# Performance work log

Measured on AMD Instinct MI355X. Metric: run time of the kernel, lower is better.

## Reference

```python
import jax, jax.numpy as jnp
import numpy as np

K = 8               # config.k
X_MIN = -1.0        # x_min
X_MAX = 1.0         # x_max
GLOBAL_COEFF = 1.0  # config.global_coeff
EPS = 1e-8          # torch cosine_similarity eps
BZ, P, D = 8192, 1024, 1024  # batch, num_pool, data_dim


def setup_inputs() -> dict:
    key = jax.random.key(0)
    k1, k2, k3, k4, k5 = jax.random.split(key, 5)
    return {
        "ppg": jax.random.normal(k1, (BZ, 1, D), dtype=jnp.float32),
        "keys_pool": jax.random.normal(k2, (P, D), dtype=jnp.float32),
        "prompt_pool": jax.random.normal(k3, (P, D), dtype=jnp.float32),
        "cnn_w": jax.random.normal(k4, (1, 1, 3), dtype=jnp.float32) * 0.5,
        "cnn_b": jax.random.normal(k5, (1,), dtype=jnp.float32) * 0.1,
    }


def _prompt_cnn(prompt, w, b):
    # PromptCNN: Conv1d(1,1,k=3,pad=1) + ReLU on [P, D]
    x = prompt[:, None, :]  # [P, 1, D]
    y = jax.lax.conv_general_dilated(
        x, w, window_strides=(1,), padding=((1, 1),),
        dimension_numbers=("NCH", "OIH", "NCH"))
    y = jax.nn.relu(y + b[None, :, None])
    return y[:, 0, :]  # [P, D]


def _global_normalizer(prompt, x_min, x_max):
    pmax = jnp.max(prompt, axis=-1, keepdims=True)
    pmin = jnp.min(prompt, axis=-1, keepdims=True)
    scale = (x_max - x_min) / (pmax - pmin)
    return scale * (prompt - pmin) + x_min


def reference(ppg, keys_pool, prompt_pool, cnn_w, cnn_b):
    # prompt pool through CNN
    pcnn = _prompt_cnn(prompt_pool, cnn_w, cnn_b)  # [P, D]

    # cosine similarity: ppg [bz,1,D] vs keys [P,D] -> [bz,P]
    pn = ppg[:, 0, :] / jnp.maximum(
        jnp.linalg.norm(ppg[:, 0, :], axis=-1, keepdims=True), EPS)
    kn = keys_pool / jnp.maximum(
        jnp.linalg.norm(keys_pool, axis=-1, keepdims=True), EPS)
    cos = jnp.einsum("bd,pd->bp", pn, kn)  # [bz, P]
    score_ = 1.0 - cos

    # top-k smallest distances (largest=False) -> ascending order
    neg_vals, idx = jax.lax.top_k(-score_, K)  # [bz, K]
    score = -neg_vals

    # entropy of softmax over raw scores
    logp = jax.nn.log_softmax(score_, axis=-1)
    entropy = -(jnp.exp(logp) * logp).sum(axis=-1).mean()

    # gather selected prompts, average over k, add singleton channel dim
    prompt = pcnn[idx].mean(axis=1)[:, None, :]  # [bz, 1, D]

    # min-max global normalization (glonorm=True)
    prompt = _global_normalizer(prompt, X_MIN, X_MAX)

    # additive combine (mul=False)
    prompted = ppg + GLOBAL_COEFF * prompt  # [bz, 1, D]

    return prompted, score.mean(), entropy
```

## Files before the change

### kernel.cpp

```cpp
#include <hip/hip_runtime.h>
#include <hip/hip_bf16.h>

#define BZ 8192
#define PP 1024
#define DD 1024
#define KSEL 8

typedef unsigned short u16;
typedef __attribute__((ext_vector_type(8))) short bf16x8;
typedef __attribute__((ext_vector_type(4))) float f32x4;

#define WS_INVK 0
#define WS_INVP 1024
#define WS_SCORE 9216
#define WS_ENT 17408
#define WS_IDX 25600
#define WS_BF16_BYTE 368640ull
#define WS_NEED (WS_BF16_BYTE + 2ull*16777216ull + 2ull*4194304ull)

__device__ __forceinline__ u16 f2bf(float x) {
  __hip_bfloat16 h = __float2bfloat16(x);
  return *(u16*)&h;
}
__device__ __forceinline__ float bf2f(u16 u) {
  __hip_bfloat16 h; *(u16*)&h = u;
  return __bfloat162float(h);
}
__device__ __forceinline__ void gll16(const void* g, void* l) {
  __builtin_amdgcn_global_load_lds((__attribute__((address_space(1))) void*)g,
                                   (__attribute__((address_space(3))) void*)l, 16, 0, 0);
}

__global__ __launch_bounds__(256) void convert_kernel(const float* __restrict__ ppg,
                                                      const float* __restrict__ keys,
                                                      float* __restrict__ ws) {
  u16* Ahi = (u16*)((char*)ws + WS_BF16_BYTE);
  u16* Alo = Ahi + 8388608;
  u16* Bhi = Alo + 8388608;
  u16* Blo = Bhi + 1048576;

  int blk = blockIdx.x;
  const float* src; u16 *hi, *lo; float* invdst;
  if (blk < PP) {
    src = keys + (size_t)blk * DD;
    hi = Bhi + (size_t)blk * DD; lo = Blo + (size_t)blk * DD;
    invdst = ws + WS_INVK + blk;
  } else {
    int r = blk - PP;
    src = ppg + (size_t)r * DD;
    hi = Ahi + (size_t)r * DD; lo = Alo + (size_t)r * DD;
    invdst = ws + WS_INVP + r;
  }
  int t = threadIdx.x;
  float4 v = ((const float4*)src)[t];
  float x[4] = {v.x, v.y, v.z, v.w};
  u16 h4[4], l4[4];
  float s = 0.f;
  #pragma unroll
  for (int j = 0; j < 4; ++j) {
    h4[j] = f2bf(x[j]);
    l4[j] = f2bf(x[j] - bf2f(h4[j]));
    s += x[j] * x[j];
  }
  *(ushort4*)(hi + t * 4) = *(ushort4*)h4;
  *(ushort4*)(lo + t * 4) = *(ushort4*)l4;

  __shared__ float red[4];
  #pragma unroll
  for (int o = 32; o > 0; o >>= 1) s += __shfl_down(s, o);
  if ((t & 63) == 0) red[t >> 6] = s;
  __syncthreads();
  if (t == 0) {
    float tot = red[0] + red[1] + red[2] + red[3];
    *invdst = 1.0f / fmaxf(sqrtf(tot), 1e-8f);
  }
}

#define LDS_AH 0
#define LDS_AL 8192
#define LDS_BH 16384
#define LDS_BL 24576

__global__ __launch_bounds__(256, 2) void gemm_mfma(const float* __restrict__ ws_ro,
                                                    float* __restrict__ C) {
  const u16* Ahi = (const u16*)((const char*)ws_ro + WS_BF16_BYTE);
  const u16* Alo = Ahi + 8388608;
  const u16* Bhi = Alo + 8388608;
  const u16* Blo = Bhi + 1048576;

  __shared__ u16 lds[32768];

  int t = threadIdx.x;
  int wid = t >> 6, lane = t & 63;
  int lr = lane & 15, lg = lane >> 4;

  int orig = blockIdx.x;
  int wg = (orig & 7) * 64 + (orig >> 3);
  int bm0 = (wg >> 3) * 128;
  int bn0 = (wg & 7) * 128;

  int wm = wid >> 1, wn = wid & 1;

  size_t offA[4], offB[4];
  int ldso[4];
  #pragma unroll
  for (int r = 0; r < 4; ++r) {
    int s = r * 256 + t;
    int row = s >> 3, g = s & 7;
    offA[r] = (size_t)(bm0 + row) * DD + g * 8;
    offB[r] = (size_t)(bn0 + row) * DD + g * 8;
    ldso[r] = (r * 256 + wid * 64) * 8;
  }

  f32x4 acc[4][4] = {};

  for (int kt = 0; kt < 16; ++kt) {
    int k0 = kt * 64;
    #pragma unroll
    for (int r = 0; r < 4; ++r) {
      gll16(Ahi + offA[r] + k0, &lds[LDS_AH + ldso[r]]);
      gll16(Alo + offA[r] + k0, &lds[LDS_AL + ldso[r]]);
      gll16(Bhi + offB[r] + k0, &lds[LDS_BH + ldso[r]]);
      gll16(Blo + offB[r] + k0, &lds[LDS_BL + ldso[r]]);
    }
    __syncthreads();

    #pragma unroll
    for (int kh = 0; kh < 2; ++kh) {
      bf16x8 ah[4], al[4], bh[4], bl[4];
      #pragma unroll
      for (int i = 0; i < 4; ++i) {
        int off = (wm * 64 + i * 16 + lr) * 64 + kh * 32 + lg * 8;
        ah[i] = *(const bf16x8*)&lds[LDS_AH + off];
        al[i] = *(const bf16x8*)&lds[LDS_AL + off];
      }
      #pragma unroll
      for (int j = 0; j < 4; ++j) {
        int off = (wn * 64 + j * 16 + lr) * 64 + kh * 32 + lg * 8;
        bh[j] = *(const bf16x8*)&lds[LDS_BH + off];
        bl[j] = *(const bf16x8*)&lds[LDS_BL + off];
      }
      #pragma unroll
      for (int i = 0; i < 4; ++i)
        #pragma unroll
        for (int j = 0; j < 4; ++j) {
          acc[i][j] = __builtin_amdgcn_mfma_f32_16x16x32_bf16(ah[i], bh[j], acc[i][j], 0, 0, 0);
          acc[i][j] = __builtin_amdgcn_mfma_f32_16x16x32_bf16(ah[i], bl[j], acc[i][j], 0, 0, 0);
          acc[i][j] = __builtin_amdgcn_mfma_f32_16x16x32_bf16(al[i], bh[j], acc[i][j], 0, 0, 0);
        }
    }
    __syncthreads();
  }

  const float* invP = ws_ro + WS_INVP;
  const float* invK = ws_ro + WS_INVK;
  #pragma unroll
  for (int i = 0; i < 4; ++i) {
    #pragma unroll
    for (int q = 0; q < 4; ++q) {
      int row = bm0 + wm * 64 + i * 16 + lg * 4 + q;
      float ip = invP[row];
      #pragma unroll
      for (int j = 0; j < 4; ++j) {
        int col = bn0 + wn * 64 + j * 16 + lr;
        C[(size_t)row * PP + col] = acc[i][j][q] * ip * invK[col];
      }
    }
  }
}

__global__ __launch_bounds__(256) void norms_kernel(const float* __restrict__ ppg,
                                                    const float* __restrict__ keys,
                                                    float* __restrict__ ws) {
  int blk = blockIdx.x;
  const float* src; float* dst;
  if (blk < PP) { src = keys + (size_t)blk * DD; dst = ws + WS_INVK + blk; }
  else          { src = ppg + (size_t)(blk - PP) * DD; dst = ws + WS_INVP + (blk - PP); }
  int t = threadIdx.x;
  float4 v = ((const float4*)src)[t];
  float s = v.x*v.x + v.y*v.y + v.z*v.z + v.w*v.w;
  __shared__ float red[4];
  #pragma unroll
  for (int o = 32; o > 0; o >>= 1) s += __shfl_down(s, o);
  if ((t & 63) == 0) red[t >> 6] = s;
  __syncthreads();
  if (t == 0) {
    float tot = red[0] + red[1] + red[2] + red[3];
    *dst = 1.0f / fmaxf(sqrtf(tot), 1e-8f);
  }
}

#define BM 128
#define BN 128
#define BK 16
__global__ __launch_bounds__(256) void gemm_kernel(const float* __restrict__ A,
                                                   const float* __restrict__ B,
                                                   const float* __restrict__ ws,
                                                   float* __restrict__ C) {
  __shared__ float As[BK][BM];
  __shared__ float Bs[BK][BN];
  int t = threadIdx.x;
  int bm0 = (blockIdx.x / (PP / BN)) * BM;
  int bn0 = (blockIdx.x % (PP / BN)) * BN;
  int tx = t & 15, ty = t >> 4;
  float acc[8][8] = {};
  int r = t & 127;
  const float* src = (t < 128) ? (A + (size_t)(bm0 + r) * DD)
                               : (B + (size_t)(bn0 + r) * DD);
  float* dstbase = (t < 128) ? &As[0][0] : &Bs[0][0];
  for (int k0 = 0; k0 < DD; k0 += BK) {
    #pragma unroll
    for (int q = 0; q < 4; ++q) {
      float4 v = *(const float4*)(src + k0 + q * 4);
      dstbase[(q * 4 + 0) * 128 + r] = v.x;
      dstbase[(q * 4 + 1) * 128 + r] = v.y;
      dstbase[(q * 4 + 2) * 128 + r] = v.z;
      dstbase[(q * 4 + 3) * 128 + r] = v.w;
    }
    __syncthreads();
    #pragma unroll
    for (int kk = 0; kk < BK; ++kk) {
      float a[8], b[8];
      *(float4*)&a[0] = *(const float4*)&As[kk][ty * 8];
      *(float4*)&a[4] = *(const float4*)&As[kk][ty * 8 + 4];
      *(float4*)&b[0] = *(const float4*)&Bs[kk][tx * 8];
      *(float4*)&b[4] = *(const float4*)&Bs[kk][tx * 8 + 4];
      #pragma unroll
      for (int i = 0; i < 8; ++i)
        #pragma unroll
        for (int j = 0; j < 8; ++j)
          acc[i][j] = fmaf(a[i], b[j], acc[i][j]);
    }
    __syncthreads();
  }
  const float* invK = ws + WS_INVK;
  const float* invP = ws + WS_INVP;
  #pragma unroll
  for (int i = 0; i < 8; ++i) {
    int row = bm0 + ty * 8 + i;
    float ia = invP[row];
    #pragma unroll
    for (int j = 0; j < 8; j += 4) {
      int col = bn0 + tx * 8 + j;
      float4 o;
      o.x = acc[i][j + 0] * ia * invK[col + 0];
      o.y = acc[i][j + 1] * ia * invK[col + 1];
      o.z = acc[i][j + 2] * ia * invK[col + 2];
      o.w = acc[i][j + 3] * ia * invK[col + 3];
      *(float4*)(C + (size_t)row * PP + col) = o;
    }
  }
}

__global__ __launch_bounds__(256) void topk_wave_kernel(const float* __restrict__ cosm,
                                                        float* __restrict__ ws) {
  int wid = threadIdx.x >> 6, lane = threadIdx.x & 63;
  int row = blockIdx.x * 4 + wid;
  const float* crow = cosm + (size_t)row * PP;

  float c[16];
  #pragma unroll
  for (int p = 0; p < 4; ++p) {
    float4 v = *(const float4*)(crow + p * 256 + lane * 4);
    c[p * 4 + 0] = v.x; c[p * 4 + 1] = v.y; c[p * 4 + 2] = v.z; c[p * 4 + 3] = v.w;
  }

  float mn = c[0];
  #pragma unroll
  for (int l = 1; l < 16; ++l) mn = fminf(mn, c[l]);
  #pragma unroll
  for (int o = 1; o < 64; o <<= 1) mn = fminf(mn, __shfl_xor(mn, o));
  float m = 1.0f - mn;

  float z = 0.f, w = 0.f;
  #pragma unroll
  for (int l = 0; l < 16; ++l) {
    float s = 1.0f - c[l];
    float e = expf(s - m);
    z += e;
    w += s * e;
  }
  #pragma unroll
  for (int o = 1; o < 64; o <<= 1) { z += __shfl_xor(z, o); w += __shfl_xor(w, o); }
  if (lane == 0) ws[WS_ENT + row] = m + logf(z) - w / z;

  unsigned used = 0;
  float score_sum = 0.f;
  int myidx = 0;
  #pragma unroll
  for (int it = 0; it < KSEL; ++it) {
    float v = -2.0f; int gi = 1 << 30;
    #pragma unroll
    for (int l = 0; l < 16; ++l) {
      if (!((used >> l) & 1u)) {
        float cv = c[l];
        int g = ((l >> 2) << 8) | (lane << 2) | (l & 3);
        if (cv > v || (cv == v && g < gi)) { v = cv; gi = g; }
      }
    }
    #pragma unroll
    for (int o = 1; o < 64; o <<= 1) {
      float ov = __shfl_xor(v, o);
      int og = __shfl_xor(gi, o);
      if (ov > v || (ov == v && og < gi)) { v = ov; gi = og; }
    }
    score_sum += 1.0f - v;
    if (((gi >> 2) & 63) == lane) used |= 1u << ((((gi >> 8) & 3) << 2) | (gi & 3));
    if (lane == it) myidx = gi;
  }
  if (lane == 0) ws[WS_SCORE + row] = score_sum;
  if (lane < KSEL) ((int*)(ws + WS_IDX))[row * KSEL + lane] = myidx;
}

__global__ __launch_bounds__(256) void prompt_kernel(const float* __restrict__ ppg,
                                                     const float* __restrict__ pool,
                                                     const float* __restrict__ cw,
                                                     const float* __restrict__ cb,
                                                     const float* __restrict__ ws,
                                                     float* __restrict__ out) {
  int row = blockIdx.x;
  int t = threadIdx.x;
  const int* idx = (const int*)(ws + WS_IDX) + row * KSEL;
  float w0 = cw[0], w1 = cw[1], w2 = cw[2], bb = cb[0];
  int d0 = t * 4;

  float a0 = 0.f, a1 = 0.f, a2 = 0.f, a3 = 0.f;
  #pragma unroll
  for (int j = 0; j < KSEL; ++j) {
    int r = idx[j];
    const float* src = pool + (size_t)r * DD;
    float4 x = *(const float4*)(src + d0);
    float xm = (d0 > 0) ? src[d0 - 1] : 0.f;
    float xp = (d0 + 4 < DD) ? src[d0 + 4] : 0.f;
    float y0 = fmaf(w0, xm,  fmaf(w1, x.x, fmaf(w2, x.y, bb)));
    float y1 = fmaf(w0, x.x, fmaf(w1, x.y, fmaf(w2, x.z, bb)));
    float y2 = fmaf(w0, x.y, fmaf(w1, x.z, fmaf(w2, x.w, bb)));
    float y3 = fmaf(w0, x.z, fmaf(w1, x.w, fmaf(w2, xp, bb)));
    a0 += fmaxf(y0, 0.f);
    a1 += fmaxf(y1, 0.f);
    a2 += fmaxf(y2, 0.f);
    a3 += fmaxf(y3, 0.f);
  }
  float p0 = a0 * 0.125f, p1 = a1 * 0.125f, p2 = a2 * 0.125f, p3 = a3 * 0.125f;

  __shared__ float rmin[4], rmax[4];
  float lmin = fminf(fminf(p0, p1), fminf(p2, p3));
  float lmax = fmaxf(fmaxf(p0, p1), fmaxf(p2, p3));
  #pragma unroll
  for (int o = 32; o > 0; o >>= 1) {
    lmin = fminf(lmin, __shfl_down(lmin, o));
    lmax = fmaxf(lmax, __shfl_down(lmax, o));
  }
  if ((t & 63) == 0) { rmin[t >> 6] = lmin; rmax[t >> 6] = lmax; }
  __syncthreads();
  float pmin = fminf(fminf(rmin[0], rmin[1]), fminf(rmin[2], rmin[3]));
  float pmax = fmaxf(fmaxf(rmax[0], rmax[1]), fmaxf(rmax[2], rmax[3]));
  float scale = 2.0f / (pmax - pmin);

  float4 pv = *(const float4*)(ppg + (size_t)row * DD + d0);
  float4 o;
  o.x = pv.x + (scale * (p0 - pmin) - 1.0f);
  o.y = pv.y + (scale * (p1 - pmin) - 1.0f);
  o.z = pv.z + (scale * (p2 - pmin) - 1.0f);
  o.w = pv.w + (scale * (p3 - pmin) - 1.0f);
  *(float4*)(out + (size_t)row * DD + d0) = o;
}

__global__ __launch_bounds__(256) void finalize_kernel(const float* __restrict__ ws,
                                                       float* __restrict__ out) {
  int t = threadIdx.x;
  const float* ss = ws + WS_SCORE;
  const float* ee = ws + WS_ENT;
  float s = 0.f, e = 0.f;
  for (int i = t; i < BZ; i += 256) { s += ss[i]; e += ee[i]; }
  __shared__ float rs[4], re[4];
  #pragma unroll
  for (int o = 32; o > 0; o >>= 1) { s += __shfl_down(s, o); e += __shfl_down(e, o); }
  if ((t & 63) == 0) { rs[t >> 6] = s; re[t >> 6] = e; }
  __syncthreads();
  if (t == 0) {
    float sT = rs[0] + rs[1] + rs[2] + rs[3];
    float eT = re[0] + re[1] + re[2] + re[3];
    out[(size_t)BZ * DD + 0] = sT / (float)(BZ * KSEL);
    out[(size_t)BZ * DD + 1] = eT / (float)BZ;
  }
}

extern "C" void kernel_launch(void* const* d_in, const int* in_sizes, int n_in,
                              void* d_out, int out_size, void* d_ws, size_t ws_size,
                              hipStream_t stream) {
  const float* ppg  = (const float*)d_in[0];
  const float* keys = (const float*)d_in[1];
  const float* pool = (const float*)d_in[2];
  const float* cw   = (const float*)d_in[3];
  const float* cb   = (const float*)d_in[4];
  float* out = (float*)d_out;
  float* ws  = (float*)d_ws;

  if (ws_size >= WS_NEED) {
    hipLaunchKernelGGL(convert_kernel, dim3(PP + BZ), dim3(256), 0, stream, ppg, keys, ws);
    hipLaunchKernelGGL(gemm_mfma, dim3((BZ / 128) * (PP / 128)), dim3(256), 0, stream, ws, out);
  } else {
    hipLaunchKernelGGL(norms_kernel, dim3(PP + BZ), dim3(256), 0, stream, ppg, keys, ws);
    hipLaunchKernelGGL(gemm_kernel, dim3((BZ / BM) * (PP / BN)), dim3(256), 0, stream,
                       ppg, keys, ws, out);
  }
  hipLaunchKernelGGL(topk_wave_kernel, dim3(BZ / 4), dim3(256), 0, stream, out, ws);
  hipLaunchKernelGGL(prompt_kernel, dim3(BZ), dim3(256), 0, stream, ppg, pool, cw, cb, ws, out);
  hipLaunchKernelGGL(finalize_kernel, dim3(1), dim3(256), 0, stream, ws, out);
}
```

Measured before the change: 146.2 us.

## Use single fp16 MFMA GEMM with pre-normalized inputs and exact fp32 top-k refinement

Replaces the three-pass bf16 hi/lo split GEMM with one fp16 MFMA pass on rows pre-normalized in the convert kernel, and writes the cosine matrix as fp16 to workspace. The top-k kernel picks 16 candidates from the approximate scores, then recomputes their exact fp32 dot products against keys and selects the final 8. This cuts MFMA work and GEMM memory traffic by about threefold, at the cost of extra gathered key reads in the top-k step. Entropy is now computed from fp16 scores with a fixed softmax shift, which trades some accuracy. The fp32 fallback path for small workspaces is removed.

```diff
diff --git a/kernel.cpp b/kernel.cpp
--- a/kernel.cpp
+++ b/kernel.cpp
@@ -6,8 +6,9 @@
 #define DD 1024
 #define KSEL 8
 
-typedef unsigned short u16;
-typedef __attribute__((ext_vector_type(8))) short bf16x8;
+typedef _Float16 f16;
+typedef __attribute__((ext_vector_type(8))) _Float16 f16x8;
+typedef __attribute__((ext_vector_type(4))) _Float16 f16x4;
 typedef __attribute__((ext_vector_type(4))) float f32x4;
 
 #define WS_INVK 0
@@ -15,80 +16,58 @@
 #define WS_SCORE 9216
 #define WS_ENT 17408
 #define WS_IDX 25600
-#define WS_BF16_BYTE 368640ull
-#define WS_NEED (WS_BF16_BYTE + 2ull*16777216ull + 2ull*4194304ull)
-
-__device__ __forceinline__ u16 f2bf(float x) {
-  __hip_bfloat16 h = __float2bfloat16(x);
-  return *(u16*)&h;
-}
-__device__ __forceinline__ float bf2f(u16 u) {
-  __hip_bfloat16 h; *(u16*)&h = u;
-  return __bfloat162float(h);
-}
+#define WS_F16_BYTE 368640ull
+#define A16_ELEMS 8388608ull
+#define B16_ELEMS 1048576ull
+
 __device__ __forceinline__ void gll16(const void* g, void* l) {
   __builtin_amdgcn_global_load_lds((__attribute__((address_space(1))) void*)g,
                                    (__attribute__((address_space(3))) void*)l, 16, 0, 0);
 }
 
-__global__ __launch_bounds__(256) void convert_kernel(const float* __restrict__ ppg,
-                                                      const float* __restrict__ keys,
-                                                      float* __restrict__ ws) {
-  u16* Ahi = (u16*)((char*)ws + WS_BF16_BYTE);
-  u16* Alo = Ahi + 8388608;
-  u16* Bhi = Alo + 8388608;
-  u16* Blo = Bhi + 1048576;
-
-  int blk = blockIdx.x;
-  const float* src; u16 *hi, *lo; float* invdst;
+__global__ __launch_bounds__(256) void convert_f16(const float* __restrict__ ppg,
+                                                   const float* __restrict__ keys,
+                                                   float* __restrict__ ws) {
+  f16* A16 = (f16*)((char*)ws + WS_F16_BYTE);
+  f16* B16 = A16 + A16_ELEMS;
+
+  int blk = blockIdx.x, t = threadIdx.x;
+  const float* src; f16* dst; float* invdst;
   if (blk < PP) {
-    src = keys + (size_t)blk * DD;
-    hi = Bhi + (size_t)blk * DD; lo = Blo + (size_t)blk * DD;
+    src = keys + (size_t)blk * DD; dst = B16 + (size_t)blk * DD;
     invdst = ws + WS_INVK + blk;
   } else {
     int r = blk - PP;
-    src = ppg + (size_t)r * DD;
-    hi = Ahi + (size_t)r * DD; lo = Alo + (size_t)r * DD;
+    src = ppg + (size_t)r * DD; dst = A16 + (size_t)r * DD;
     invdst = ws + WS_INVP + r;
   }
-  int t = threadIdx.x;
   float4 v = ((const float4*)src)[t];
   float x[4] = {v.x, v.y, v.z, v.w};
-  u16 h4[4], l4[4];
-  float s = 0.f;
-  #pragma unroll
-  for (int j = 0; j < 4; ++j) {
-    h4[j] = f2bf(x[j]);
-    l4[j] = f2bf(x[j] - bf2f(h4[j]));
-    s += x[j] * x[j];
-  }
-  *(ushort4*)(hi + t * 4) = *(ushort4*)h4;
-  *(ushort4*)(lo + t * 4) = *(ushort4*)l4;
-
+  float s = x[0]*x[0] + x[1]*x[1] + x[2]*x[2] + x[3]*x[3];
   __shared__ float red[4];
   #pragma unroll
   for (int o = 32; o > 0; o >>= 1) s += __shfl_down(s, o);
   if ((t & 63) == 0) red[t >> 6] = s;
   __syncthreads();
-  if (t == 0) {
-    float tot = red[0] + red[1] + red[2] + red[3];
-    *invdst = 1.0f / fmaxf(sqrtf(tot), 1e-8f);
-  }
-}
-
-#define LDS_AH 0
-#define LDS_AL 8192
-#define LDS_BH 16384
-#define LDS_BL 24576
-
-__global__ __launch_bounds__(256, 2) void gemm_mfma(const float* __restrict__ ws_ro,
-                                                    float* __restrict__ C) {
-  const u16* Ahi = (const u16*)((const char*)ws_ro + WS_BF16_BYTE);
-  const u16* Alo = Ahi + 8388608;
-  const u16* Bhi = Alo + 8388608;
-  const u16* Blo = Bhi + 1048576;
-
-  __shared__ u16 lds[32768];
+  float tot = red[0] + red[1] + red[2] + red[3];
+  float inv = 1.0f / fmaxf(sqrtf(tot), 1e-8f);
+  f16x4 h;
+  #pragma unroll
+  for (int j = 0; j < 4; ++j) h[j] = (_Float16)(x[j] * inv);
+  *(f16x4*)(dst + t * 4) = h;
+  if (t == 0) *invdst = inv;
+}
+
+#define LDS_A 0
+#define LDS_B 8192
+
+__global__ __launch_bounds__(256, 2) void gemm_f16(const float* __restrict__ ws_ro,
+                                                   float* __restrict__ ws_w) {
+  const f16* A16 = (const f16*)((const char*)ws_ro + WS_F16_BYTE);
+  const f16* B16 = A16 + A16_ELEMS;
+  f16* C16 = (f16*)((char*)ws_w + WS_F16_BYTE) + A16_ELEMS + B16_ELEMS;
+
+  __shared__ unsigned short lds[16384];
 
   int t = threadIdx.x;
   int wid = t >> 6, lane = t & 63;
@@ -98,7 +77,6 @@
   int wg = (orig & 7) * 64 + (orig >> 3);
   int bm0 = (wg >> 3) * 128;
   int bn0 = (wg & 7) * 128;
-
   int wm = wid >> 1, wn = wid & 1;
 
   size_t offA[4], offB[4];
@@ -118,183 +96,81 @@
     int k0 = kt * 64;
     #pragma unroll
     for (int r = 0; r < 4; ++r) {
-      gll16(Ahi + offA[r] + k0, &lds[LDS_AH + ldso[r]]);
-      gll16(Alo + offA[r] + k0, &lds[LDS_AL + ldso[r]]);
-      gll16(Bhi + offB[r] + k0, &lds[LDS_BH + ldso[r]]);
-      gll16(Blo + offB[r] + k0, &lds[LDS_BL + ldso[r]]);
+      gll16(A16 + offA[r] + k0, &lds[LDS_A + ldso[r]]);
+      gll16(B16 + offB[r] + k0, &lds[LDS_B + ldso[r]]);
     }
     __syncthreads();
 
     #pragma unroll
     for (int kh = 0; kh < 2; ++kh) {
-      bf16x8 ah[4], al[4], bh[4], bl[4];
+      f16x8 af[4], bf[4];
       #pragma unroll
       for (int i = 0; i < 4; ++i) {
         int off = (wm * 64 + i * 16 + lr) * 64 + kh * 32 + lg * 8;
-        ah[i] = *(const bf16x8*)&lds[LDS_AH + off];
-        al[i] = *(const bf16x8*)&lds[LDS_AL + off];
+        af[i] = *(const f16x8*)&lds[LDS_A + off];
       }
       #pragma unroll
       for (int j = 0; j < 4; ++j) {
         int off = (wn * 64 + j * 16 + lr) * 64 + kh * 32 + lg * 8;
-        bh[j] = *(const bf16x8*)&lds[LDS_BH + off];
-        bl[j] = *(const bf16x8*)&lds[LDS_BL + off];
+        bf[j] = *(const f16x8*)&lds[LDS_B + off];
       }
       #pragma unroll
       for (int i = 0; i < 4; ++i)
         #pragma unroll
-        for (int j = 0; j < 4; ++j) {
-          acc[i][j] = __builtin_amdgcn_mfma_f32_16x16x32_bf16(ah[i], bh[j], acc[i][j], 0, 0, 0);
-          acc[i][j] = __builtin_amdgcn_mfma_f32_16x16x32_bf16(ah[i], bl[j], acc[i][j], 0, 0, 0);
-          acc[i][j] = __builtin_amdgcn_mfma_f32_16x16x32_bf16(al[i], bh[j], acc[i][j], 0, 0, 0);
-        }
+        for (int j = 0; j < 4; ++j)
+          acc[i][j] = __builtin_amdgcn_mfma_f32_16x16x32_f16(af[i], bf[j], acc[i][j], 0, 0, 0);
     }
     __syncthreads();
   }
 
-  const float* invP = ws_ro + WS_INVP;
-  const float* invK = ws_ro + WS_INVK;
-  #pragma unroll
-  for (int i = 0; i < 4; ++i) {
+  #pragma unroll
+  for (int i = 0; i < 4; ++i)
     #pragma unroll
     for (int q = 0; q < 4; ++q) {
       int row = bm0 + wm * 64 + i * 16 + lg * 4 + q;
-      float ip = invP[row];
       #pragma unroll
       for (int j = 0; j < 4; ++j) {
         int col = bn0 + wn * 64 + j * 16 + lr;
-        C[(size_t)row * PP + col] = acc[i][j][q] * ip * invK[col];
-      }
-    }
-  }
-}
-
-__global__ __launch_bounds__(256) void norms_kernel(const float* __restrict__ ppg,
-                                                    const float* __restrict__ keys,
-                                                    float* __restrict__ ws) {
-  int blk = blockIdx.x;
-  const float* src; float* dst;
-  if (blk < PP) { src = keys + (size_t)blk * DD; dst = ws + WS_INVK + blk; }
-  else          { src = ppg + (size_t)(blk - PP) * DD; dst = ws + WS_INVP + (blk - PP); }
-  int t = threadIdx.x;
-  float4 v = ((const float4*)src)[t];
-  float s = v.x*v.x + v.y*v.y + v.z*v.z + v.w*v.w;
-  __shared__ float red[4];
-  #pragma unroll
-  for (int o = 32; o > 0; o >>= 1) s += __shfl_down(s, o);
-  if ((t & 63) == 0) red[t >> 6] = s;
-  __syncthreads();
-  if (t == 0) {
-    float tot = red[0] + red[1] + red[2] + red[3];
-    *dst = 1.0f / fmaxf(sqrtf(tot), 1e-8f);
-  }
-}
-
-#define BM 128
-#define BN 128
-#define BK 16
-__global__ __launch_bounds__(256) void gemm_kernel(const float* __restrict__ A,
-                                                   const float* __restrict__ B,
-                                                   const float* __restrict__ ws,
-                                                   float* __restrict__ C) {
-  __shared__ float As[BK][BM];
-  __shared__ float Bs[BK][BN];
-  int t = threadIdx.x;
-  int bm0 = (blockIdx.x / (PP / BN)) * BM;
-  int bn0 = (blockIdx.x % (PP / BN)) * BN;
-  int tx = t & 15, ty = t >> 4;
-  float acc[8][8] = {};
-  int r = t & 127;
-  const float* src = (t < 128) ? (A + (size_t)(bm0 + r) * DD)
-                               : (B + (size_t)(bn0 + r) * DD);
-  float* dstbase = (t < 128) ? &As[0][0] : &Bs[0][0];
-  for (int k0 = 0; k0 < DD; k0 += BK) {
-    #pragma unroll
-    for (int q = 0; q < 4; ++q) {
-      float4 v = *(const float4*)(src + k0 + q * 4);
-      dstbase[(q * 4 + 0) * 128 + r] = v.x;
-      dstbase[(q * 4 + 1) * 128 + r] = v.y;
-      dstbase[(q * 4 + 2) * 128 + r] = v.z;
-      dstbase[(q * 4 + 3) * 128 + r] = v.w;
-    }
-    __syncthreads();
-    #pragma unroll
-    for (int kk = 0; kk < BK; ++kk) {
-      float a[8], b[8];
-      *(float4*)&a[0] = *(const float4*)&As[kk][ty * 8];
-      *(float4*)&a[4] = *(const float4*)&As[kk][ty * 8 + 4];
-      *(float4*)&b[0] = *(const float4*)&Bs[kk][tx * 8];
-      *(float4*)&b[4] = *(const float4*)&Bs[kk][tx * 8 + 4];
-      #pragma unroll
-      for (int i = 0; i < 8; ++i)
-        #pragma unroll
-        for (int j = 0; j < 8; ++j)
-          acc[i][j] = fmaf(a[i], b[j], acc[i][j]);
-    }
-    __syncthreads();
-  }
-  const float* invK = ws + WS_INVK;
-  const float* invP = ws + WS_INVP;
-  #pragma unroll
-  for (int i = 0; i < 8; ++i) {
-    int row = bm0 + ty * 8 + i;
-    float ia = invP[row];
-    #pragma unroll
-    for (int j = 0; j < 8; j += 4) {
-      int col = bn0 + tx * 8 + j;
-      float4 o;
-      o.x = acc[i][j + 0] * ia * invK[col + 0];
-      o.y = acc[i][j + 1] * ia * invK[col + 1];
-      o.z = acc[i][j + 2] * ia * invK[col + 2];
-      o.w = acc[i][j + 3] * ia * invK[col + 3];
-      *(float4*)(C + (size_t)row * PP + col) = o;
-    }
-  }
-}
-
-__global__ __launch_bounds__(256) void topk_wave_kernel(const float* __restrict__ cosm,
-                                                        float* __restrict__ ws) {
+        C16[(size_t)row * PP + col] = (_Float16)acc[i][j][q];
+      }
+    }
+}
+
+__global__ __launch_bounds__(256) void topk_refine(const float* __restrict__ ppg,
+                                                   const float* __restrict__ keys,
+                                                   float* __restrict__ ws) {
+  const f16* C16 = (const f16*)((const char*)ws + WS_F16_BYTE) + A16_ELEMS + B16_ELEMS;
   int wid = threadIdx.x >> 6, lane = threadIdx.x & 63;
   int row = blockIdx.x * 4 + wid;
-  const float* crow = cosm + (size_t)row * PP;
-
+  const f16* crow = C16 + (size_t)row * PP;
+
+  f16x8 va = *(const f16x8*)(crow + lane * 16);
+  f16x8 vb = *(const f16x8*)(crow + lane * 16 + 8);
   float c[16];
   #pragma unroll
-  for (int p = 0; p < 4; ++p) {
-    float4 v = *(const float4*)(crow + p * 256 + lane * 4);
-    c[p * 4 + 0] = v.x; c[p * 4 + 1] = v.y; c[p * 4 + 2] = v.z; c[p * 4 + 3] = v.w;
-  }
-
-  float mn = c[0];
-  #pragma unroll
-  for (int l = 1; l < 16; ++l) mn = fminf(mn, c[l]);
-  #pragma unroll
-  for (int o = 1; o < 64; o <<= 1) mn = fminf(mn, __shfl_xor(mn, o));
-  float m = 1.0f - mn;
+  for (int j = 0; j < 8; ++j) { c[j] = (float)va[j]; c[8 + j] = (float)vb[j]; }
 
   float z = 0.f, w = 0.f;
   #pragma unroll
   for (int l = 0; l < 16; ++l) {
     float s = 1.0f - c[l];
-    float e = expf(s - m);
-    z += e;
-    w += s * e;
+    float e = __expf(s - 2.0f);
+    z += e; w += s * e;
   }
   #pragma unroll
   for (int o = 1; o < 64; o <<= 1) { z += __shfl_xor(z, o); w += __shfl_xor(w, o); }
-  if (lane == 0) ws[WS_ENT + row] = m + logf(z) - w / z;
+  if (lane == 0) ws[WS_ENT + row] = 2.0f + __logf(z) - w / z;
 
   unsigned used = 0;
-  float score_sum = 0.f;
-  int myidx = 0;
-  #pragma unroll
-  for (int it = 0; it < KSEL; ++it) {
+  int cand = 0;
+  #pragma unroll
+  for (int it = 0; it < 16; ++it) {
     float v = -2.0f; int gi = 1 << 30;
     #pragma unroll
     for (int l = 0; l < 16; ++l) {
       if (!((used >> l) & 1u)) {
         float cv = c[l];
-        int g = ((l >> 2) << 8) | (lane << 2) | (l & 3);
+        int g = lane * 16 + l;
         if (cv > v || (cv == v && g < gi)) { v = cv; gi = g; }
       }
     }
@@ -304,12 +180,56 @@
       int og = __shfl_xor(gi, o);
       if (ov > v || (ov == v && og < gi)) { v = ov; gi = og; }
     }
-    score_sum += 1.0f - v;
-    if (((gi >> 2) & 63) == lane) used |= 1u << ((((gi >> 8) & 3) << 2) | (gi & 3));
-    if (lane == it) myidx = gi;
-  }
-  if (lane == 0) ws[WS_SCORE + row] = score_sum;
-  if (lane < KSEL) ((int*)(ws + WS_IDX))[row * KSEL + lane] = myidx;
+    if ((gi >> 4) == lane) used |= 1u << (gi & 15);
+    if (lane == it) cand = gi;
+  }
+
+  float p[16];
+  const float* prow = ppg + (size_t)row * DD;
+  #pragma unroll
+  for (int q = 0; q < 4; ++q) {
+    float4 pv = *(const float4*)(prow + lane * 16 + q * 4);
+    p[q * 4 + 0] = pv.x; p[q * 4 + 1] = pv.y; p[q * 4 + 2] = pv.z; p[q * 4 + 3] = pv.w;
+  }
+  float ip = ws[WS_INVP + row];
+  float rc[16]; int cd[16];
+  #pragma unroll 4
+  for (int tt = 0; tt < 16; ++tt) {
+    int bc = __shfl(cand, tt);
+    cd[tt] = bc;
+    const float* krow = keys + (size_t)bc * DD;
+    float d = 0.f;
+    #pragma unroll
+    for (int q = 0; q < 4; ++q) {
+      float4 kv = *(const float4*)(krow + lane * 16 + q * 4);
+      d = fmaf(p[q * 4 + 0], kv.x, d);
+      d = fmaf(p[q * 4 + 1], kv.y, d);
+      d = fmaf(p[q * 4 + 2], kv.z, d);
+      d = fmaf(p[q * 4 + 3], kv.w, d);
+    }
+    #pragma unroll
+    for (int o = 1; o < 64; o <<= 1) d += __shfl_xor(d, o);
+    rc[tt] = d * ip * ws[WS_INVK + bc];
+  }
+
+  unsigned u2 = 0;
+  float ssum = 0.f;
+  int mysel = 0;
+  #pragma unroll
+  for (int it = 0; it < KSEL; ++it) {
+    float bv = -2.0f; int bt = 0, bci = 1 << 30;
+    #pragma unroll
+    for (int tt = 0; tt < 16; ++tt) {
+      if (!((u2 >> tt) & 1u)) {
+        if (rc[tt] > bv || (rc[tt] == bv && cd[tt] < bci)) { bv = rc[tt]; bt = tt; bci = cd[tt]; }
+      }
+    }
+    ssum += 1.0f - bv;
+    u2 |= 1u << bt;
+    if (lane == it) mysel = bci;
+  }
+  if (lane == 0) ws[WS_SCORE + row] = ssum;
+  if (lane < KSEL) ((int*)(ws + WS_IDX))[row * KSEL + lane] = mysel;
 }
 
 __global__ __launch_bounds__(256) void prompt_kernel(const float* __restrict__ ppg,
@@ -397,15 +317,9 @@
   float* out = (float*)d_out;
   float* ws  = (float*)d_ws;
 
-  if (ws_size >= WS_NEED) {
-    hipLaunchKernelGGL(convert_kernel, dim3(PP + BZ), dim3(256), 0, stream, ppg, keys, ws);
-    hipLaunchKernelGGL(gemm_mfma, dim3((BZ / 128) * (PP / 128)), dim3(256), 0, stream, ws, out);
-  } else {
-    hipLaunchKernelGGL(norms_kernel, dim3(PP + BZ), dim3(256), 0, stream, ppg, keys, ws);
-    hipLaunchKernelGGL(gemm_kernel, dim3((BZ / BM) * (PP / BN)), dim3(256), 0, stream,
-                       ppg, keys, ws, out);
-  }
-  hipLaunchKernelGGL(topk_wave_kernel, dim3(BZ / 4), dim3(256), 0, stream, out, ws);
+  hipLaunchKernelGGL(convert_f16, dim3(PP + BZ), dim3(256), 0, stream, ppg, keys, ws);
+  hipLaunchKernelGGL(gemm_f16, dim3((BZ / 128) * (PP / 128)), dim3(256), 0, stream, ws, ws);
+  hipLaunchKernelGGL(topk_refine, dim3(BZ / 4), dim3(256), 0, stream, ppg, keys, ws);
   hipLaunchKernelGGL(prompt_kernel, dim3(BZ), dim3(256), 0, stream, ppg, pool, cw, cb, ws, out);
   hipLaunchKernelGGL(finalize_kernel, dim3(1), dim3(256), 0, stream, ws, out);
 }
```

Result: slower. 206.0 us (+40.9%).

## Fuse top-k and prompt gather into one wave-per-row kernel

Applied to the files above, without the earlier changes.

Merges the top-k/entropy kernel and the prompt CNN/normalize kernel into a single kernel where each wave handles one row and passes the selected indices by shuffle instead of through workspace memory. The entropy pass drops its row-min reduction and uses a fixed shift of 2 with fast exp/log intrinsics, which relies on cosine being at least -1. The fallback fp32 GEMM path and the workspace-size check are removed, so the MFMA path now runs unconditionally. This removes one launch and the index round trip, at the cost of more registers per wave and in-place reuse of the cos rows in out.

```diff
diff --git a/kernel.cpp b/kernel.cpp
--- a/kernel.cpp
+++ b/kernel.cpp
@@ -14,9 +14,7 @@
 #define WS_INVP 1024
 #define WS_SCORE 9216
 #define WS_ENT 17408
-#define WS_IDX 25600
 #define WS_BF16_BYTE 368640ull
-#define WS_NEED (WS_BF16_BYTE + 2ull*16777216ull + 2ull*4194304ull)
 
 __device__ __forceinline__ u16 f2bf(float x) {
   __hip_bfloat16 h = __float2bfloat16(x);
@@ -98,7 +96,6 @@
   int wg = (orig & 7) * 64 + (orig >> 3);
   int bm0 = (wg >> 3) * 128;
   int bn0 = (wg & 7) * 128;
-
   int wm = wid >> 1, wn = wid & 1;
 
   size_t offA[4], offB[4];
@@ -169,120 +166,33 @@
   }
 }
 
-__global__ __launch_bounds__(256) void norms_kernel(const float* __restrict__ ppg,
-                                                    const float* __restrict__ keys,
-                                                    float* __restrict__ ws) {
-  int blk = blockIdx.x;
-  const float* src; float* dst;
-  if (blk < PP) { src = keys + (size_t)blk * DD; dst = ws + WS_INVK + blk; }
-  else          { src = ppg + (size_t)(blk - PP) * DD; dst = ws + WS_INVP + (blk - PP); }
-  int t = threadIdx.x;
-  float4 v = ((const float4*)src)[t];
-  float s = v.x*v.x + v.y*v.y + v.z*v.z + v.w*v.w;
-  __shared__ float red[4];
-  #pragma unroll
-  for (int o = 32; o > 0; o >>= 1) s += __shfl_down(s, o);
-  if ((t & 63) == 0) red[t >> 6] = s;
-  __syncthreads();
-  if (t == 0) {
-    float tot = red[0] + red[1] + red[2] + red[3];
-    *dst = 1.0f / fmaxf(sqrtf(tot), 1e-8f);
-  }
-}
-
-#define BM 128
-#define BN 128
-#define BK 16
-__global__ __launch_bounds__(256) void gemm_kernel(const float* __restrict__ A,
-                                                   const float* __restrict__ B,
-                                                   const float* __restrict__ ws,
-                                                   float* __restrict__ C) {
-  __shared__ float As[BK][BM];
-  __shared__ float Bs[BK][BN];
-  int t = threadIdx.x;
-  int bm0 = (blockIdx.x / (PP / BN)) * BM;
-  int bn0 = (blockIdx.x % (PP / BN)) * BN;
-  int tx = t & 15, ty = t >> 4;
-  float acc[8][8] = {};
-  int r = t & 127;
-  const float* src = (t < 128) ? (A + (size_t)(bm0 + r) * DD)
-                               : (B + (size_t)(bn0 + r) * DD);
-  float* dstbase = (t < 128) ? &As[0][0] : &Bs[0][0];
-  for (int k0 = 0; k0 < DD; k0 += BK) {
-    #pragma unroll
-    for (int q = 0; q < 4; ++q) {
-      float4 v = *(const float4*)(src + k0 + q * 4);
-      dstbase[(q * 4 + 0) * 128 + r] = v.x;
-      dstbase[(q * 4 + 1) * 128 + r] = v.y;
-      dstbase[(q * 4 + 2) * 128 + r] = v.z;
-      dstbase[(q * 4 + 3) * 128 + r] = v.w;
-    }
-    __syncthreads();
-    #pragma unroll
-    for (int kk = 0; kk < BK; ++kk) {
-      float a[8], b[8];
-      *(float4*)&a[0] = *(const float4*)&As[kk][ty * 8];
-      *(float4*)&a[4] = *(const float4*)&As[kk][ty * 8 + 4];
-      *(float4*)&b[0] = *(const float4*)&Bs[kk][tx * 8];
-      *(float4*)&b[4] = *(const float4*)&Bs[kk][tx * 8 + 4];
-      #pragma unroll
-      for (int i = 0; i < 8; ++i)
-        #pragma unroll
-        for (int j = 0; j < 8; ++j)
-          acc[i][j] = fmaf(a[i], b[j], acc[i][j]);
-    }
-    __syncthreads();
-  }
-  const float* invK = ws + WS_INVK;
-  const float* invP = ws + WS_INVP;
-  #pragma unroll
-  for (int i = 0; i < 8; ++i) {
-    int row = bm0 + ty * 8 + i;
-    float ia = invP[row];
-    #pragma unroll
-    for (int j = 0; j < 8; j += 4) {
-      int col = bn0 + tx * 8 + j;
-      float4 o;
-      o.x = acc[i][j + 0] * ia * invK[col + 0];
-      o.y = acc[i][j + 1] * ia * invK[col + 1];
-      o.z = acc[i][j + 2] * ia * invK[col + 2];
-      o.w = acc[i][j + 3] * ia * invK[col + 3];
-      *(float4*)(C + (size_t)row * PP + col) = o;
-    }
-  }
-}
-
-__global__ __launch_bounds__(256) void topk_wave_kernel(const float* __restrict__ cosm,
-                                                        float* __restrict__ ws) {
+__global__ __launch_bounds__(256) void fused_wave_topk_prompt(
+    const float* __restrict__ ppg, const float* __restrict__ pool,
+    const float* __restrict__ cw, const float* __restrict__ cb,
+    float* __restrict__ ws, float* __restrict__ out) {
   int wid = threadIdx.x >> 6, lane = threadIdx.x & 63;
   int row = blockIdx.x * 4 + wid;
-  const float* crow = cosm + (size_t)row * PP;
+  const float* crow = out + (size_t)row * PP;
 
   float c[16];
   #pragma unroll
   for (int p = 0; p < 4; ++p) {
-    float4 v = *(const float4*)(crow + p * 256 + lane * 4);
-    c[p * 4 + 0] = v.x; c[p * 4 + 1] = v.y; c[p * 4 + 2] = v.z; c[p * 4 + 3] = v.w;
-  }
-
-  float mn = c[0];
-  #pragma unroll
-  for (int l = 1; l < 16; ++l) mn = fminf(mn, c[l]);
-  #pragma unroll
-  for (int o = 1; o < 64; o <<= 1) mn = fminf(mn, __shfl_xor(mn, o));
-  float m = 1.0f - mn;
-
-  float z = 0.f, w = 0.f;
-  #pragma unroll
-  for (int l = 0; l < 16; ++l) {
-    float s = 1.0f - c[l];
-    float e = expf(s - m);
-    z += e;
-    w += s * e;
-  }
-  #pragma unroll
-  for (int o = 1; o < 64; o <<= 1) { z += __shfl_xor(z, o); w += __shfl_xor(w, o); }
-  if (lane == 0) ws[WS_ENT + row] = m + logf(z) - w / z;
+    f32x4 v = *(const f32x4*)(crow + p * 256 + lane * 4);
+    c[p * 4 + 0] = v[0]; c[p * 4 + 1] = v[1]; c[p * 4 + 2] = v[2]; c[p * 4 + 3] = v[3];
+  }
+
+  {
+    float z = 0.f, w = 0.f;
+    #pragma unroll
+    for (int l = 0; l < 16; ++l) {
+      float s = 1.0f - c[l];
+      float e = __expf(s - 2.0f);
+      z += e; w += s * e;
+    }
+    #pragma unroll
+    for (int o = 1; o < 64; o <<= 1) { z += __shfl_xor(z, o); w += __shfl_xor(w, o); }
+    if (lane == 0) ws[WS_ENT + row] = 2.0f + __logf(z) - w / z;
+  }
 
   unsigned used = 0;
   float score_sum = 0.f;
@@ -309,61 +219,57 @@
     if (lane == it) myidx = gi;
   }
   if (lane == 0) ws[WS_SCORE + row] = score_sum;
-  if (lane < KSEL) ((int*)(ws + WS_IDX))[row * KSEL + lane] = myidx;
-}
-
-__global__ __launch_bounds__(256) void prompt_kernel(const float* __restrict__ ppg,
-                                                     const float* __restrict__ pool,
-                                                     const float* __restrict__ cw,
-                                                     const float* __restrict__ cb,
-                                                     const float* __restrict__ ws,
-                                                     float* __restrict__ out) {
-  int row = blockIdx.x;
-  int t = threadIdx.x;
-  const int* idx = (const int*)(ws + WS_IDX) + row * KSEL;
+
+  const float* prow = ppg + (size_t)row * DD;
+  f32x4 pv[4];
+  #pragma unroll
+  for (int j = 0; j < 4; ++j)
+    pv[j] = *(const f32x4*)(prow + j * 256 + lane * 4);
+
   float w0 = cw[0], w1 = cw[1], w2 = cw[2], bb = cb[0];
-  int d0 = t * 4;
-
-  float a0 = 0.f, a1 = 0.f, a2 = 0.f, a3 = 0.f;
-  #pragma unroll
-  for (int j = 0; j < KSEL; ++j) {
-    int r = idx[j];
-    const float* src = pool + (size_t)r * DD;
-    float4 x = *(const float4*)(src + d0);
-    float xm = (d0 > 0) ? src[d0 - 1] : 0.f;
-    float xp = (d0 + 4 < DD) ? src[d0 + 4] : 0.f;
-    float y0 = fmaf(w0, xm,  fmaf(w1, x.x, fmaf(w2, x.y, bb)));
-    float y1 = fmaf(w0, x.x, fmaf(w1, x.y, fmaf(w2, x.z, bb)));
-    float y2 = fmaf(w0, x.y, fmaf(w1, x.z, fmaf(w2, x.w, bb)));
-    float y3 = fmaf(w0, x.z, fmaf(w1, x.w, fmaf(w2, xp, bb)));
-    a0 += fmaxf(y0, 0.f);
-    a1 += fmaxf(y1, 0.f);
-    a2 += fmaxf(y2, 0.f);
-    a3 += fmaxf(y3, 0.f);
-  }
-  float p0 = a0 * 0.125f, p1 = a1 * 0.125f, p2 = a2 * 0.125f, p3 = a3 * 0.125f;
-
-  __shared__ float rmin[4], rmax[4];
-  float lmin = fminf(fminf(p0, p1), fminf(p2, p3));
-  float lmax = fmaxf(fmaxf(p0, p1), fmaxf(p2, p3));
-  #pragma unroll
-  for (int o = 32; o > 0; o >>= 1) {
-    lmin = fminf(lmin, __shfl_down(lmin, o));
-    lmax = fmaxf(lmax, __shfl_down(lmax, o));
-  }
-  if ((t & 63) == 0) { rmin[t >> 6] = lmin; rmax[t >> 6] = lmax; }
-  __syncthreads();
-  float pmin = fminf(fminf(rmin[0], rmin[1]), fminf(rmin[2], rmin[3]));
-  float pmax = fmaxf(fmaxf(rmax[0], rmax[1]), fmaxf(rmax[2], rmax[3]));
-  float scale = 2.0f / (pmax - pmin);
-
-  float4 pv = *(const float4*)(ppg + (size_t)row * DD + d0);
-  float4 o;
-  o.x = pv.x + (scale * (p0 - pmin) - 1.0f);
-  o.y = pv.y + (scale * (p1 - pmin) - 1.0f);
-  o.z = pv.z + (scale * (p2 - pmin) - 1.0f);
-  o.w = pv.w + (scale * (p3 - pmin) - 1.0f);
-  *(float4*)(out + (size_t)row * DD + d0) = o;
+  float a[16] = {};
+  #pragma unroll
+  for (int s = 0; s < KSEL; ++s) {
+    int rj = __shfl(myidx, s);
+    const float* src = pool + (size_t)rj * DD;
+    #pragma unroll
+    for (int j = 0; j < 4; ++j) {
+      int d0 = j * 256 + lane * 4;
+      f32x4 x = *(const f32x4*)(src + d0);
+      float xm = (d0 > 0) ? src[d0 - 1] : 0.f;
+      float xp = (d0 + 4 < DD) ? src[d0 + 4] : 0.f;
+      float y0 = fmaf(w0, xm,   fmaf(w1, x[0], fmaf(w2, x[1], bb)));
+      float y1 = fmaf(w0, x[0], fmaf(w1, x[1], fmaf(w2, x[2], bb)));
+      float y2 = fmaf(w0, x[1], fmaf(w1, x[2], fmaf(w2, x[3], bb)));
+      float y3 = fmaf(w0, x[2], fmaf(w1, x[3], fmaf(w2, xp,   bb)));
+      a[j * 4 + 0] += fmaxf(y0, 0.f);
+      a[j * 4 + 1] += fmaxf(y1, 0.f);
+      a[j * 4 + 2] += fmaxf(y2, 0.f);
+      a[j * 4 + 3] += fmaxf(y3, 0.f);
+    }
+  }
+  #pragma unroll
+  for (int l = 0; l < 16; ++l) a[l] *= 0.125f;
+
+  float lmin = a[0], lmax = a[0];
+  #pragma unroll
+  for (int l = 1; l < 16; ++l) { lmin = fminf(lmin, a[l]); lmax = fmaxf(lmax, a[l]); }
+  #pragma unroll
+  for (int o = 1; o < 64; o <<= 1) {
+    lmin = fminf(lmin, __shfl_xor(lmin, o));
+    lmax = fmaxf(lmax, __shfl_xor(lmax, o));
+  }
+  float scale = 2.0f / (lmax - lmin);
+
+  float* orow = out + (size_t)row * DD;
+  #pragma unroll
+  for (int j = 0; j < 4; ++j) {
+    f32x4 o4;
+    #pragma unroll
+    for (int q = 0; q < 4; ++q)
+      o4[q] = pv[j][q] + (scale * (a[j * 4 + q] - lmin) - 1.0f);
+    *(f32x4*)(orow + j * 256 + lane * 4) = o4;
+  }
 }
 
 __global__ __launch_bounds__(256) void finalize_kernel(const float* __restrict__ ws,
@@ -397,15 +303,9 @@
   float* out = (float*)d_out;
   float* ws  = (float*)d_ws;
 
-  if (ws_size >= WS_NEED) {
-    hipLaunchKernelGGL(convert_kernel, dim3(PP + BZ), dim3(256), 0, stream, ppg, keys, ws);
-    hipLaunchKernelGGL(gemm_mfma, dim3((BZ / 128) * (PP / 128)), dim3(256), 0, stream, ws, out);
-  } else {
-    hipLaunchKernelGGL(norms_kernel, dim3(PP + BZ), dim3(256), 0, stream, ppg, keys, ws);
-    hipLaunchKernelGGL(gemm_kernel, dim3((BZ / BM) * (PP / BN)), dim3(256), 0, stream,
-                       ppg, keys, ws, out);
-  }
-  hipLaunchKernelGGL(topk_wave_kernel, dim3(BZ / 4), dim3(256), 0, stream, out, ws);
-  hipLaunchKernelGGL(prompt_kernel, dim3(BZ), dim3(256), 0, stream, ppg, pool, cw, cb, ws, out);
+  hipLaunchKernelGGL(convert_kernel, dim3(PP + BZ), dim3(256), 0, stream, ppg, keys, ws);
+  hipLaunchKernelGGL(gemm_mfma, dim3((BZ / 128) * (PP / 128)), dim3(256), 0, stream, ws, out);
+  hipLaunchKernelGGL(fused_wave_topk_prompt, dim3(BZ / 4), dim3(256), 0, stream,
+                     ppg, pool, cw, cb, ws, out);
   hipLaunchKernelGGL(finalize_kernel, dim3(1), dim3(256), 0, stream, ws, out);
 }
```

Measured after the change: 153.4 us. 5.0% more time.
